# Performance work log

Hardware: AMD Instinct MI355X
Metric: run time of the kernel (lower is better)

Reference implementation:

```python
import jax, jax.numpy as jnp
import numpy as np

B, N, E = 64, 256, 2048          # graphs per batch, nodes per subgraph, edges per subgraph
V, D, H = 50000, 128, 4          # vocab_size, hidden_dim, heads
NEG_SLOPE = 0.2                  # PyG GATConv default LeakyReLU slope


def setup_inputs() -> dict:
    key = jax.random.key(0)
    ks = jax.random.split(key, 16)
    s = 0.05
    return {
        "neighbors_node1": jax.random.randint(ks[0], (B, N), 0, V),
        "neighbors_node2": jax.random.randint(ks[1], (B, N), 0, V),
        "adj1": jax.random.randint(ks[2], (B, 2, E), 0, N),
        "adj2": jax.random.randint(ks[3], (B, 2, E), 0, N),
        "emb": jax.random.normal(ks[4], (V + 1, D), jnp.float32) * 0.02,
        # GATConv 1: lin weight [H*D, D], att_src/att_dst [H, D], bias [D] (concat=False)
        "W1": jax.random.normal(ks[5], (H * D, D), jnp.float32) * s,
        "att_src1": jax.random.normal(ks[6], (H, D), jnp.float32) * s,
        "att_dst1": jax.random.normal(ks[7], (H, D), jnp.float32) * s,
        "b1": jnp.zeros((D,), jnp.float32),
        # GATConv 2
        "W2": jax.random.normal(ks[8], (H * D, D), jnp.float32) * s,
        "att_src2": jax.random.normal(ks[9], (H, D), jnp.float32) * s,
        "att_dst2": jax.random.normal(ks[10], (H, D), jnp.float32) * s,
        "b2": jnp.zeros((D,), jnp.float32),
        # final MLP: Linear(2D -> 1)
        "mlp_w": jax.random.normal(ks[11], (1, 2 * D), jnp.float32) * s,
        "mlp_b": jnp.zeros((1,), jnp.float32),
    }


def _gat_conv(x, edge_index, W, a_src, a_dst, bias):
    """PyG GATConv, concat=False (mean over heads), with self-loops.
    x: [N, D] node features; edge_index: [2, E] (row=src j, col=dst i)."""
    xh = (x @ W.T).reshape(N, H, D)                      # [N, H, D]
    loop = jnp.arange(N)
    src = jnp.concatenate([edge_index[0], loop])          # [E+N]
    dst = jnp.concatenate([edge_index[1], loop])
    asrc = jnp.einsum('nhd,hd->nh', xh, a_src)            # [N, H]
    adst = jnp.einsum('nhd,hd->nh', xh, a_dst)
    e = jax.nn.leaky_relu(asrc[src] + adst[dst], NEG_SLOPE)   # [E+N, H]
    # softmax over incoming edges of each dst node
    m = jax.ops.segment_max(e, dst, num_segments=N)
    ex = jnp.exp(e - m[dst])
    denom = jax.ops.segment_sum(ex, dst, num_segments=N)
    alpha = ex / denom[dst]                               # [E+N, H]
    out = jax.ops.segment_sum(xh[src] * alpha[:, :, None], dst, num_segments=N)  # [N, H, D]
    return out.mean(axis=1) + bias                        # [N, D]


def reference(neighbors_node1, neighbors_node2, adj1, adj2, emb,
              W1, att_src1, att_dst1, b1,
              W2, att_src2, att_dst2, b2,
              mlp_w, mlp_b):
    f1 = jax.vmap(lambda n, ei: _gat_conv(emb[n], ei, W1, att_src1, att_dst1, b1))(
        neighbors_node1, adj1)                            # [B, N, D]
    f2 = jax.vmap(lambda n, ei: _gat_conv(emb[n], ei, W2, att_src2, att_dst2, b2))(
        neighbors_node2, adj2)
    feats = jnp.concatenate([f1[:, 0], f2[:, 0]], axis=-1)  # center node of each subgraph -> [B, 2D]
    return (feats @ mlp_w.T + mlp_b)[:, 0]                # [B]
```

## Files before the change

kernel.cpp:

```cpp
#include <hip/hip_runtime.h>
#include <hip/hip_bf16.h>

#define Bg 64
#define Nn 256
#define Ee 2048
#define Dd 128
#define Hh 4
#define MAXJ 40
#define RS 132

__device__ __forceinline__ float bf2f(unsigned short u) {
    return __uint_as_float(((unsigned)u) << 16);
}

__global__ __launch_bounds__(256) void precompute_kernel(
    const void* W1, const void* as1, const void* ad1, const void* b1,
    const void* W2, const void* as2, const void* ad2, const void* b2,
    const void* mlpw, const void* mlpb, float* wv)
{
    __shared__ float s_av[3 * Dd];
    __shared__ float s_part[8 * 3 * Dd];
    __shared__ float s_red[2];
    __shared__ int   s_f32;

    const int tid = threadIdx.x;
    const int x = blockIdx.x;
    const int l = x >> 2, h = x & 3;

    if (tid < 64) {
        float v = bf2f(((const unsigned short*)W1)[tid]);
        bool bad = !(v > -64.f && v < 64.f);
        unsigned long long m = __ballot(bad);
        if (tid == 0) s_f32 = (m != 0ull) ? 1 : 0;
    }
    __syncthreads();
    const int f32 = s_f32;

    for (int i = tid; i < 3 * Dd; i += 256) {
        int t = i >> 7, d = i & 127;
        const void* p; long off;
        if (t == 0)      { p = l ? as2 : as1; off = (long)h * Dd + d; }
        else if (t == 1) { p = l ? ad2 : ad1; off = (long)h * Dd + d; }
        else             { p = mlpw;          off = (long)l * Dd + d; }
        s_av[i] = f32 ? ((const float*)p)[off]
                      : bf2f(((const unsigned short*)p)[off]);
    }
    __syncthreads();

    {
        const int kc = (tid & 31) * 4;
        const int d0 = (tid >> 5) * 16;
        float acc[3][4] = {};
        if (f32) {
            const float* Wf = (const float*)(l ? W2 : W1) + (long)h * Dd * Dd;
            #pragma unroll
            for (int dd = 0; dd < 16; ++dd) {
                int d = d0 + dd;
                float4 w = *(const float4*)(Wf + (long)d * Dd + kc);
                #pragma unroll
                for (int t = 0; t < 3; ++t) {
                    float a = s_av[t * Dd + d];
                    acc[t][0] += a * w.x; acc[t][1] += a * w.y;
                    acc[t][2] += a * w.z; acc[t][3] += a * w.w;
                }
            }
        } else {
            const unsigned short* Wb =
                (const unsigned short*)(l ? W2 : W1) + (long)h * Dd * Dd;
            #pragma unroll
            for (int dd = 0; dd < 16; ++dd) {
                int d = d0 + dd;
                ushort4 u = *(const ushort4*)(Wb + (long)d * Dd + kc);
                float wx = bf2f(u.x), wy = bf2f(u.y);
                float wz = bf2f(u.z), ww = bf2f(u.w);
                #pragma unroll
                for (int t = 0; t < 3; ++t) {
                    float a = s_av[t * Dd + d];
                    acc[t][0] += a * wx; acc[t][1] += a * wy;
                    acc[t][2] += a * wz; acc[t][3] += a * ww;
                }
            }
        }
        const int dg = tid >> 5;
        #pragma unroll
        for (int t = 0; t < 3; ++t)
            *(float4*)&s_part[(dg * 3 + t) * Dd + kc] =
                make_float4(acc[t][0], acc[t][1], acc[t][2], acc[t][3]);
    }
    __syncthreads();

    for (int i = tid; i < 3 * Dd; i += 256) {
        int t = i >> 7, k = i & 127;
        float s = 0.f;
        #pragma unroll
        for (int g = 0; g < 8; ++g) s += s_part[(g * 3 + t) * Dd + k];
        wv[((l * 3 + t) * 4 + h) * Dd + k] = s;
    }

    if (h == 0) {
        float p = 0.f;
        if (tid < 128) {
            const void* bias = l ? b2 : b1;
            float bv = f32 ? ((const float*)bias)[tid]
                           : bf2f(((const unsigned short*)bias)[tid]);
            p = bv * s_av[2 * Dd + tid];
        }
        #pragma unroll
        for (int off = 32; off > 0; off >>= 1) p += __shfl_down(p, off);
        if (tid == 0 || tid == 64) s_red[tid >> 6] = p;
        __syncthreads();
        if (tid == 0) {
            float a = s_red[0] + s_red[1];
            if (l == 0) a += f32 ? ((const float*)mlpb)[0]
                                 : bf2f(((const unsigned short*)mlpb)[0]);
            wv[3072 + l] = a;
        }
    }
}

__global__ __launch_bounds__(512) void gat_main_kernel(
    const int* nn1, const int* nn2, const int* adj1, const int* adj2,
    const void* emb, const void* W1, const float* wv, void* out)
{
    __shared__ float s_wv[24 * RS];
    __shared__ float s_rows[2 * MAXJ * RS];
    __shared__ int   s_nodes[2][Nn];
    __shared__ int   s_srcj[2][MAXJ];
    __shared__ int   s_gid[2 * MAXJ];
    __shared__ int   s_cnt[2];
    __shared__ int   s_f32;
    __shared__ float s_ps[2 * MAXJ * Hh], s_pm[2 * MAXJ * Hh];
    __shared__ float s_pd[2 * Hh], s_hval[2 * Hh], s_bdot[2];

    const int tid = threadIdx.x;
    const int b = blockIdx.x;

    if (tid == 0) { s_cnt[0] = 0; s_cnt[1] = 0; }
    if (tid < 64) {
        float v = bf2f(((const unsigned short*)W1)[tid]);
        bool bad = !(v > -64.f && v < 64.f);
        unsigned long long m = __ballot(bad);
        if (tid == 0) s_f32 = (m != 0ull) ? 1 : 0;
    }
    __syncthreads();
    const int f32 = s_f32;

    for (int v = tid; v < 2 * (Ee / 4); v += 512) {
        int l = v >> 9, i = v & 511;
        const int* adjp = (l ? adj2 : adj1) + (long)b * 2 * Ee;
        int4 d4 = ((const int4*)(adjp + Ee))[i];
        int base = i * 4;
        if (d4.x == 0) { int p = atomicAdd(&s_cnt[l], 1); if (p < MAXJ - 1) s_srcj[l][p] = adjp[base + 0]; }
        if (d4.y == 0) { int p = atomicAdd(&s_cnt[l], 1); if (p < MAXJ - 1) s_srcj[l][p] = adjp[base + 1]; }
        if (d4.z == 0) { int p = atomicAdd(&s_cnt[l], 1); if (p < MAXJ - 1) s_srcj[l][p] = adjp[base + 2]; }
        if (d4.w == 0) { int p = atomicAdd(&s_cnt[l], 1); if (p < MAXJ - 1) s_srcj[l][p] = adjp[base + 3]; }
    }
    {
        int l = tid >> 8, n = tid & 255;
        s_nodes[l][n] = (l ? nn2 : nn1)[b * Nn + n];
    }
    for (int i = tid; i < 768; i += 512) {
        float4 f = ((const float4*)wv)[i];
        int el = i * 4, row = el >> 7, k = el & 127;
        *(float4*)&s_wv[row * RS + k] = f;
    }
    if (tid < 2) s_bdot[tid] = wv[3072 + tid];
    __syncthreads();

    if (tid < 2) {
        int c = s_cnt[tid];
        if (c > MAXJ - 1) c = MAXJ - 1;
        s_srcj[tid][c] = 0;
        s_cnt[tid] = c + 1;
    }
    __syncthreads();
    const int cnt0 = s_cnt[0], cnt1 = s_cnt[1];
    const int tot = cnt0 + cnt1;

    if (tid < 2 * MAXJ) {
        int l = tid / MAXJ, j = tid % MAXJ;
        int cl = l ? cnt1 : cnt0;
        if (j < cl) s_gid[l ? (cnt0 + j) : j] = s_nodes[l][s_srcj[l][j]];
    }
    __syncthreads();

    if (f32) {
        for (int idx = tid; idx < tot * 32; idx += 512) {
            int j = idx >> 5, k4 = (idx & 31) << 2;
            long gid = s_gid[j];
            float4 f = ((const float4*)emb)[gid * 32 + (k4 >> 2)];
            *(float4*)&s_rows[j * RS + k4] = f;
        }
    } else {
        for (int idx = tid; idx < tot * 16; idx += 512) {
            int j = idx >> 4, k8 = (idx & 15) << 3;
            long gid = s_gid[j];
            uint4 u = *(const uint4*)((const unsigned short*)emb + gid * Dd + k8);
            float4 f0 = make_float4(bf2f(u.x & 0xffff), bf2f(u.x >> 16),
                                    bf2f(u.y & 0xffff), bf2f(u.y >> 16));
            float4 f1 = make_float4(bf2f(u.z & 0xffff), bf2f(u.z >> 16),
                                    bf2f(u.w & 0xffff), bf2f(u.w >> 16));
            *(float4*)&s_rows[j * RS + k8] = f0;
            *(float4*)&s_rows[j * RS + k8 + 4] = f1;
        }
    }
    __syncthreads();

    const int ntask = tot * 8 + 8;
    for (int task = tid; task < ntask; task += 512) {
        int j, h, t, l;
        if (task < tot * 8) {
            j = task >> 3; h = (task >> 1) & 3; t = (task & 1) ? 2 : 0;
            l = (j < cnt0) ? 0 : 1;
        } else {
            int z = task - tot * 8;
            l = z >> 2; h = z & 3; t = 1;
            j = l ? (tot - 1) : (cnt0 - 1);
        }
        const float* wrow = s_wv + ((l * 3 + t) * 4 + h) * RS;
        const float* row  = s_rows + j * RS;
        float acc = 0.f;
        #pragma unroll 8
        for (int k = 0; k < Dd; ++k) acc += row[k] * wrow[k];
        if (task < tot * 8) {
            if (task & 1) s_pm[j * Hh + h] = acc;
            else          s_ps[j * Hh + h] = acc;
        } else {
            s_pd[(l << 2) | h] = acc;
        }
    }
    __syncthreads();

    if (tid < 8) {
        int l = tid >> 2, h = tid & 3;
        int j0 = l ? cnt0 : 0;
        int j1 = l ? tot : cnt0;
        float pd = s_pd[tid], m = -1e30f;
        for (int j = j0; j < j1; ++j) {
            float e = s_ps[j * Hh + h] + pd;
            e = (e >= 0.f) ? e : 0.2f * e;
            s_ps[j * Hh + h] = e;
            if (e > m) m = e;
        }
        float den = 0.f, num = 0.f;
        for (int j = j0; j < j1; ++j) {
            float ex = expf(s_ps[j * Hh + h] - m);
            den += ex;
            num += ex * s_pm[j * Hh + h];
        }
        s_hval[tid] = num / den;
    }
    __syncthreads();
    if (tid == 0) {
        float r = 0.25f * (s_hval[0] + s_hval[1] + s_hval[2] + s_hval[3]) + s_bdot[0]
                + 0.25f * (s_hval[4] + s_hval[5] + s_hval[6] + s_hval[7]) + s_bdot[1];
        if (f32) ((float*)out)[b] = r;
        else     ((__hip_bfloat16*)out)[b] = __float2bfloat16(r);
    }
}

extern "C" void kernel_launch(void* const* d_in, const int* in_sizes, int n_in,
                              void* d_out, int out_size, void* d_ws, size_t ws_size,
                              hipStream_t stream) {
    const int* nn1  = (const int*)d_in[0];
    const int* nn2  = (const int*)d_in[1];
    const int* adj1 = (const int*)d_in[2];
    const int* adj2 = (const int*)d_in[3];
    float* wv = (float*)d_ws;

    precompute_kernel<<<8, 256, 0, stream>>>(
        d_in[5],   d_in[6],   d_in[7],
        d_in[8],
        d_in[9],   d_in[10],  d_in[11],
        d_in[12],
        d_in[13],  d_in[14],  wv);

    gat_main_kernel<<<Bg, 512, 0, stream>>>(
        nn1, nn2, adj1, adj2, d_in[4] , d_in[5] , wv, d_out);
}
```

Before: 104.3 us.

## Split precompute across more blocks, drop gather barriers, vectorise dot products

The precompute kernel now launches 32 blocks, each covering a quarter of the output columns, so the weight matrices are streamed by more CUs in parallel. The main kernel drops the s_gid staging pass and two __syncthreads, working out the gather node id inline with the self-loop entry handled implicitly. The per-task dot products read float4 from shared memory, and __restrict__ is added to the pointers. The cost is more index arithmetic per gather element and a longer 32-way partial-sum reduction in each precompute block.

```diff
diff --git a/kernel.cpp b/kernel.cpp
--- a/kernel.cpp
+++ b/kernel.cpp
@@ -14,28 +14,29 @@
 }
 
 __global__ __launch_bounds__(256) void precompute_kernel(
-    const void* W1, const void* as1, const void* ad1, const void* b1,
-    const void* W2, const void* as2, const void* ad2, const void* b2,
-    const void* mlpw, const void* mlpb, float* wv)
+    const void* __restrict__ W1, const void* __restrict__ as1,
+    const void* __restrict__ ad1, const void* __restrict__ b1,
+    const void* __restrict__ W2, const void* __restrict__ as2,
+    const void* __restrict__ ad2, const void* __restrict__ b2,
+    const void* __restrict__ mlpw, const void* __restrict__ mlpb,
+    float* __restrict__ wv)
 {
     __shared__ float s_av[3 * Dd];
-    __shared__ float s_part[8 * 3 * Dd];
+    __shared__ float s_part[32 * 3 * 32];
     __shared__ float s_red[2];
     __shared__ int   s_f32;
 
     const int tid = threadIdx.x;
     const int x = blockIdx.x;
-    const int l = x >> 2, h = x & 3;
+    const int l = x >> 4, h = (x >> 2) & 3, q = x & 3;
 
     if (tid < 64) {
         float v = bf2f(((const unsigned short*)W1)[tid]);
-        bool bad = !(v > -64.f && v < 64.f);
-        unsigned long long m = __ballot(bad);
+        unsigned long long m = __ballot(!(v > -64.f && v < 64.f));
         if (tid == 0) s_f32 = (m != 0ull) ? 1 : 0;
     }
     __syncthreads();
     const int f32 = s_f32;
-
     for (int i = tid; i < 3 * Dd; i += 256) {
         int t = i >> 7, d = i & 127;
         const void* p; long off;
@@ -48,15 +49,16 @@
     __syncthreads();
 
     {
-        const int kc = (tid & 31) * 4;
-        const int d0 = (tid >> 5) * 16;
+        const int c4 = (tid & 7) * 4;
+        const int dg = tid >> 3;
+        const int k0 = q * 32 + c4;
         float acc[3][4] = {};
         if (f32) {
             const float* Wf = (const float*)(l ? W2 : W1) + (long)h * Dd * Dd;
             #pragma unroll
-            for (int dd = 0; dd < 16; ++dd) {
-                int d = d0 + dd;
-                float4 w = *(const float4*)(Wf + (long)d * Dd + kc);
+            for (int dd = 0; dd < 4; ++dd) {
+                int d = dg * 4 + dd;
+                float4 w = *(const float4*)(Wf + (long)d * Dd + k0);
                 #pragma unroll
                 for (int t = 0; t < 3; ++t) {
                     float a = s_av[t * Dd + d];
@@ -68,9 +70,9 @@
             const unsigned short* Wb =
                 (const unsigned short*)(l ? W2 : W1) + (long)h * Dd * Dd;
             #pragma unroll
-            for (int dd = 0; dd < 16; ++dd) {
-                int d = d0 + dd;
-                ushort4 u = *(const ushort4*)(Wb + (long)d * Dd + kc);
+            for (int dd = 0; dd < 4; ++dd) {
+                int d = dg * 4 + dd;
+                ushort4 u = *(const ushort4*)(Wb + (long)d * Dd + k0);
                 float wx = bf2f(u.x), wy = bf2f(u.y);
                 float wz = bf2f(u.z), ww = bf2f(u.w);
                 #pragma unroll
@@ -81,23 +83,22 @@
                 }
             }
         }
-        const int dg = tid >> 5;
         #pragma unroll
         for (int t = 0; t < 3; ++t)
-            *(float4*)&s_part[(dg * 3 + t) * Dd + kc] =
+            *(float4*)&s_part[(dg * 3 + t) * 32 + c4] =
                 make_float4(acc[t][0], acc[t][1], acc[t][2], acc[t][3]);
     }
     __syncthreads();
 
-    for (int i = tid; i < 3 * Dd; i += 256) {
-        int t = i >> 7, k = i & 127;
+    if (tid < 96) {
+        int t = tid >> 5, c = tid & 31;
         float s = 0.f;
         #pragma unroll
-        for (int g = 0; g < 8; ++g) s += s_part[(g * 3 + t) * Dd + k];
-        wv[((l * 3 + t) * 4 + h) * Dd + k] = s;
-    }
-
-    if (h == 0) {
+        for (int g = 0; g < 32; ++g) s += s_part[(g * 3 + t) * 32 + c];
+        wv[((l * 3 + t) * 4 + h) * Dd + q * 32 + c] = s;
+    }
+
+    if (h == 0 && q == 0) {
         float p = 0.f;
         if (tid < 128) {
             const void* bias = l ? b2 : b1;
@@ -119,14 +120,15 @@
 }
 
 __global__ __launch_bounds__(512) void gat_main_kernel(
-    const int* nn1, const int* nn2, const int* adj1, const int* adj2,
-    const void* emb, const void* W1, const float* wv, void* out)
+    const int* __restrict__ nn1, const int* __restrict__ nn2,
+    const int* __restrict__ adj1, const int* __restrict__ adj2,
+    const void* __restrict__ emb, const void* __restrict__ W1,
+    const float* __restrict__ wv, void* __restrict__ out)
 {
     __shared__ float s_wv[24 * RS];
     __shared__ float s_rows[2 * MAXJ * RS];
     __shared__ int   s_nodes[2][Nn];
     __shared__ int   s_srcj[2][MAXJ];
-    __shared__ int   s_gid[2 * MAXJ];
     __shared__ int   s_cnt[2];
     __shared__ int   s_f32;
     __shared__ float s_ps[2 * MAXJ * Hh], s_pm[2 * MAXJ * Hh];
@@ -138,8 +140,7 @@
     if (tid == 0) { s_cnt[0] = 0; s_cnt[1] = 0; }
     if (tid < 64) {
         float v = bf2f(((const unsigned short*)W1)[tid]);
-        bool bad = !(v > -64.f && v < 64.f);
-        unsigned long long m = __ballot(bad);
+        unsigned long long m = __ballot(!(v > -64.f && v < 64.f));
         if (tid == 0) s_f32 = (m != 0ull) ? 1 : 0;
     }
     __syncthreads();
@@ -167,34 +168,29 @@
     if (tid < 2) s_bdot[tid] = wv[3072 + tid];
     __syncthreads();
 
-    if (tid < 2) {
-        int c = s_cnt[tid];
-        if (c > MAXJ - 1) c = MAXJ - 1;
-        s_srcj[tid][c] = 0;
-        s_cnt[tid] = c + 1;
-    }
-    __syncthreads();
-    const int cnt0 = s_cnt[0], cnt1 = s_cnt[1];
+    const int cnt0 = min(s_cnt[0], MAXJ - 1) + 1;
+    const int cnt1 = min(s_cnt[1], MAXJ - 1) + 1;
     const int tot = cnt0 + cnt1;
-
-    if (tid < 2 * MAXJ) {
-        int l = tid / MAXJ, j = tid % MAXJ;
-        int cl = l ? cnt1 : cnt0;
-        if (j < cl) s_gid[l ? (cnt0 + j) : j] = s_nodes[l][s_srcj[l][j]];
-    }
-    __syncthreads();
 
     if (f32) {
         for (int idx = tid; idx < tot * 32; idx += 512) {
             int j = idx >> 5, k4 = (idx & 31) << 2;
-            long gid = s_gid[j];
+            int l = (j < cnt0) ? 0 : 1;
+            int jj = l ? (j - cnt0) : j;
+            int cl = l ? cnt1 : cnt0;
+            int src = (jj == cl - 1) ? 0 : s_srcj[l][jj];
+            long gid = s_nodes[l][src];
             float4 f = ((const float4*)emb)[gid * 32 + (k4 >> 2)];
             *(float4*)&s_rows[j * RS + k4] = f;
         }
     } else {
         for (int idx = tid; idx < tot * 16; idx += 512) {
             int j = idx >> 4, k8 = (idx & 15) << 3;
-            long gid = s_gid[j];
+            int l = (j < cnt0) ? 0 : 1;
+            int jj = l ? (j - cnt0) : j;
+            int cl = l ? cnt1 : cnt0;
+            int src = (jj == cl - 1) ? 0 : s_srcj[l][jj];
+            long gid = s_nodes[l][src];
             uint4 u = *(const uint4*)((const unsigned short*)emb + gid * Dd + k8);
             float4 f0 = make_float4(bf2f(u.x & 0xffff), bf2f(u.x >> 16),
                                     bf2f(u.y & 0xffff), bf2f(u.y >> 16));
@@ -217,11 +213,14 @@
             l = z >> 2; h = z & 3; t = 1;
             j = l ? (tot - 1) : (cnt0 - 1);
         }
-        const float* wrow = s_wv + ((l * 3 + t) * 4 + h) * RS;
-        const float* row  = s_rows + j * RS;
+        const float4* w4 = (const float4*)(s_wv + ((l * 3 + t) * 4 + h) * RS);
+        const float4* r4 = (const float4*)(s_rows + j * RS);
         float acc = 0.f;
         #pragma unroll 8
-        for (int k = 0; k < Dd; ++k) acc += row[k] * wrow[k];
+        for (int k = 0; k < Dd / 4; ++k) {
+            float4 a = r4[k], w = w4[k];
+            acc += a.x * w.x + a.y * w.y + a.z * w.z + a.w * w.w;
+        }
         if (task < tot * 8) {
             if (task & 1) s_pm[j * Hh + h] = acc;
             else          s_ps[j * Hh + h] = acc;
@@ -268,7 +267,7 @@
     const int* adj2 = (const int*)d_in[3];
     float* wv = (float*)d_ws;
 
-    precompute_kernel<<<8, 256, 0, stream>>>(
+    precompute_kernel<<<32, 256, 0, stream>>>(
         d_in[5],   d_in[6],   d_in[7],
         d_in[8],
         d_in[9],   d_in[10],  d_in[11],
```

Result: slower. 107.6 us (+3.2%).
